# Performance work log

Measured on AMD Instinct MI355X. Metric: run time of the kernel, lower is better.

The kernel has to match this reference:

```python
import jax, jax.numpy as jnp
import numpy as np

B = 2048
D = 256
TEMPERATURE = 0.5
EPS = 1e-8  # torch.nn.CosineSimilarity eps


def _neg_indices(b):
    # Static mask: exclude diagonal and positive pairs (i, B+i), (B+i, i).
    n = 2 * b
    mask = np.ones((n, n), dtype=bool)
    np.fill_diagonal(mask, False)
    idx = np.arange(b)
    mask[idx, b + idx] = False
    mask[b + idx, idx] = False
    rows, cols = np.nonzero(mask)  # row-major order, matches torch sim[mask]
    return rows.reshape(n, n - 2), cols.reshape(n, n - 2)

_NEG_ROWS, _NEG_COLS = _neg_indices(B)


def setup_inputs() -> dict:
    key = jax.random.key(0)
    k1, k2 = jax.random.split(key)
    z_i = jax.random.normal(k1, (B, D), dtype=jnp.float32)
    z_j = jax.random.normal(k2, (B, D), dtype=jnp.float32)
    return {"z_i": z_i, "z_j": z_j}


def reference(z_i, z_j):
    b = z_i.shape[0]
    n = 2 * b
    z = jnp.concatenate([z_i, z_j], axis=0)  # [N, D]
    # Cosine similarity = normalize -> matmul (same math as broadcast CosineSimilarity)
    norm = jnp.maximum(jnp.linalg.norm(z, axis=1, keepdims=True), EPS)
    zn = z / norm
    sim = (zn @ zn.T) / TEMPERATURE  # [N, N]
    # positives: diag(sim, B) and diag(sim, -B)
    pos = jnp.concatenate([jnp.diagonal(sim, offset=b), jnp.diagonal(sim, offset=-b)], axis=0)  # [N]
    # negatives: static masked gather -> [N, N-2]
    neg = sim[_NEG_ROWS, _NEG_COLS]
    logits = jnp.concatenate([pos[:, None], neg], axis=1)  # [N, N-1]
    # CrossEntropyLoss(reduction='sum') with labels all zero, then / N
    loss = -jax.nn.log_softmax(logits, axis=1)[:, 0]
    return jnp.sum(loss) / n
```

## Files before the change

### kernel.cpp

```cpp
#include <hip/hip_runtime.h>
#include <hip/hip_bf16.h>
#include <math.h>

#define B_PAIRS 2048
#define N_ROWS  4096
#define D_DIM   256
#define INV_T   2.0f

typedef __attribute__((ext_vector_type(8))) short  short8;
typedef __attribute__((ext_vector_type(4))) float  floatx4;


__device__ __forceinline__ void async_copy16(const void* gsrc, void* ldst) {
    __builtin_amdgcn_global_load_lds(
        (__attribute__((address_space(1))) void*)gsrc,
        (__attribute__((address_space(3))) void*)ldst,
        16, 0, 0);
}

__global__ void ntx_normalize(const float* __restrict__ z_i,
                              const float* __restrict__ z_j,
                              __hip_bfloat16* __restrict__ zn) {
    const int row = blockIdx.x;
    const int tid = threadIdx.x;
    const float* src = (row < B_PAIRS) ? (z_i + (size_t)row * D_DIM)
                                       : (z_j + (size_t)(row - B_PAIRS) * D_DIM);
    float v  = src[tid];
    float ss = v * v;
    #pragma unroll
    for (int off = 32; off > 0; off >>= 1) ss += __shfl_down(ss, off, 64);
    __shared__ float red[4];
    const int lane = tid & 63, w = tid >> 6;
    if (lane == 0) red[w] = ss;
    __syncthreads();
    if (tid == 0) red[0] = red[0] + red[1] + red[2] + red[3];
    __syncthreads();
    float norm = fmaxf(sqrtf(red[0]), 1e-8f);
    zn[(size_t)row * D_DIM + tid] = __float2bfloat16(v / norm);
}

#define BM 128
#define BN 128
#define BK 32

__global__ __launch_bounds__(256)
void ntx_simtile(const __hip_bfloat16* __restrict__ zn,
                 float* __restrict__ S,
                 float* __restrict__ pos) {
    __shared__ __align__(16) __hip_bfloat16 As[BM * BK];
    __shared__ __align__(16) __hip_bfloat16 Bs[BN * BK];

    const int tid  = threadIdx.x;
    const int lane = tid & 63;
    const int w    = tid >> 6;
    const int wr   = w >> 1;
    const int wc   = w & 1;
    const int quad = lane >> 4;
    const int l16  = lane & 15;

    const int rowA0 = blockIdx.y * BM;
    const int rowB0 = blockIdx.x * BN;

    floatx4 acc[4][4];
    #pragma unroll
    for (int i = 0; i < 4; i++)
        #pragma unroll
        for (int j = 0; j < 4; j++)
            acc[i][j] = (floatx4){0.f, 0.f, 0.f, 0.f};

    for (int k0 = 0; k0 < D_DIM; k0 += BK) {
        #pragma unroll
        for (int c = 0; c < 2; c++) {
            const int chunk = tid + c * 256;
            const int r  = chunk >> 2;
            const int kc = chunk & 3;
            async_copy16(zn + ((size_t)(rowA0 + r) * D_DIM + k0 + kc * 8),
                         As + chunk * 8);
            async_copy16(zn + ((size_t)(rowB0 + r) * D_DIM + k0 + kc * 8),
                         Bs + chunk * 8);
        }
        __syncthreads();

        short8 afr[4], bfr[4];
        #pragma unroll
        for (int fi = 0; fi < 4; fi++) {
            const int ar = wr * 64 + fi * 16 + l16;
            afr[fi] = *(const short8*)(const void*)(As + ar * BK + quad * 8);
        }
        #pragma unroll
        for (int fj = 0; fj < 4; fj++) {
            const int brw = wc * 64 + fj * 16 + l16;
            bfr[fj] = *(const short8*)(const void*)(Bs + brw * BK + quad * 8);
        }
        #pragma unroll
        for (int fi = 0; fi < 4; fi++)
            #pragma unroll
            for (int fj = 0; fj < 4; fj++)
                acc[fi][fj] = __builtin_amdgcn_mfma_f32_16x16x32_bf16(
                    afr[fi], bfr[fj], acc[fi][fj], 0, 0, 0);
        __syncthreads();
    }

    #pragma unroll
    for (int fi = 0; fi < 4; fi++) {
        float rs[4] = {0.f, 0.f, 0.f, 0.f};
        #pragma unroll
        for (int fj = 0; fj < 4; fj++) {
            const int jg = rowB0 + wc * 64 + fj * 16 + l16;
            #pragma unroll
            for (int reg = 0; reg < 4; reg++) {
                const int ig = rowA0 + wr * 64 + fi * 16 + quad * 4 + reg;
                const float v = acc[fi][fj][reg] * INV_T;
                if (jg == (ig ^ B_PAIRS)) pos[ig] = v;
                rs[reg] += (jg == ig) ? 0.f : __expf(v);
            }
        }
        #pragma unroll
        for (int reg = 0; reg < 4; reg++) {
            float r = rs[reg];
            r += __shfl_xor(r, 1, 16);
            r += __shfl_xor(r, 2, 16);
            r += __shfl_xor(r, 4, 16);
            r += __shfl_xor(r, 8, 16);
            if (l16 == 0) {
                const int ig = rowA0 + wr * 64 + fi * 16 + quad * 4 + reg;
                atomicAdd(&S[ig], r);
            }
        }
    }
}

__global__ void ntx_finalize(const float* __restrict__ S,
                             const float* __restrict__ pos,
                             float* __restrict__ out) {
    const int tid = threadIdx.x;
    float acc = 0.f;
    for (int i = tid; i < N_ROWS; i += 256)
        acc += logf(S[i]) - pos[i];
    #pragma unroll
    for (int off = 32; off > 0; off >>= 1) acc += __shfl_down(acc, off, 64);
    __shared__ float red[4];
    if ((tid & 63) == 0) red[tid >> 6] = acc;
    __syncthreads();
    if (tid == 0)
        out[0] = (red[0] + red[1] + red[2] + red[3]) / (float)N_ROWS;
}

extern "C" void kernel_launch(void* const* d_in, const int* in_sizes, int n_in,
                              void* d_out, int out_size, void* d_ws, size_t ws_size,
                              hipStream_t stream) {
    const float* z_i = (const float*)d_in[0];
    const float* z_j = (const float*)d_in[1];
    float* out = (float*)d_out;

    __hip_bfloat16* zn = (__hip_bfloat16*)d_ws;
    float* S   = (float*)((char*)d_ws + (size_t)N_ROWS * D_DIM * sizeof(__hip_bfloat16));
    float* pos = S + N_ROWS;

    hipMemsetAsync(S, 0, N_ROWS * sizeof(float), stream);

    ntx_normalize<<<N_ROWS, D_DIM, 0, stream>>>(z_i, z_j, zn);

    dim3 grid(N_ROWS / BN, N_ROWS / BM);
    ntx_simtile<<<grid, 256, 0, stream>>>(zn, S, pos);

    ntx_finalize<<<1, 256, 0, stream>>>(S, pos, out);
}
```

Before: 94.56 us.

## Exploit similarity symmetry with upper-triangular tiles and fold memset into normalize

The similarity tile kernel now runs only the 528 upper-triangular tiles of the symmetric sim matrix. Each off-diagonal tile adds its exp values to both the row sums and the column sums, which roughly halves the MFMA and exp work. The normalize kernel handles one row per wavefront with float4 loads and also zeroes S, so the separate memset launch is gone. Finalize uses 1024 threads and fast log. The costs are more atomics per tile (column sums on top of row sums) and a serial loop at block start that decodes the tile index.

Result: faster. 81.48 us (-13.8%).

```diff
diff --git a/kernel.cpp b/kernel.cpp
--- a/kernel.cpp
+++ b/kernel.cpp
@@ -18,30 +18,34 @@
         16, 0, 0);
 }
 
-__global__ void ntx_normalize(const float* __restrict__ z_i,
-                              const float* __restrict__ z_j,
-                              __hip_bfloat16* __restrict__ zn) {
-    const int row = blockIdx.x;
-    const int tid = threadIdx.x;
+__global__ __launch_bounds__(256)
+void ntx_normalize(const float* __restrict__ z_i,
+                   const float* __restrict__ z_j,
+                   __hip_bfloat16* __restrict__ zn,
+                   float* __restrict__ S) {
+    const int w    = threadIdx.x >> 6;
+    const int lane = threadIdx.x & 63;
+    const int row  = blockIdx.x * 4 + w;
     const float* src = (row < B_PAIRS) ? (z_i + (size_t)row * D_DIM)
                                        : (z_j + (size_t)(row - B_PAIRS) * D_DIM);
-    float v  = src[tid];
-    float ss = v * v;
+    const float4 v = *(const float4*)(src + lane * 4);
+    float ss = v.x * v.x + v.y * v.y + v.z * v.z + v.w * v.w;
     #pragma unroll
-    for (int off = 32; off > 0; off >>= 1) ss += __shfl_down(ss, off, 64);
-    __shared__ float red[4];
-    const int lane = tid & 63, w = tid >> 6;
-    if (lane == 0) red[w] = ss;
-    __syncthreads();
-    if (tid == 0) red[0] = red[0] + red[1] + red[2] + red[3];
-    __syncthreads();
-    float norm = fmaxf(sqrtf(red[0]), 1e-8f);
-    zn[(size_t)row * D_DIM + tid] = __float2bfloat16(v / norm);
+    for (int off = 32; off > 0; off >>= 1) ss += __shfl_xor(ss, off, 64);
+    const float rn = 1.0f / fmaxf(sqrtf(ss), 1e-8f);
+    union { short4 s4; __hip_bfloat16 h[4]; } u;
+    u.h[0] = __float2bfloat16(v.x * rn);
+    u.h[1] = __float2bfloat16(v.y * rn);
+    u.h[2] = __float2bfloat16(v.z * rn);
+    u.h[3] = __float2bfloat16(v.w * rn);
+    *(short4*)(void*)(zn + (size_t)row * D_DIM + lane * 4) = u.s4;
+    if (lane == 0) S[row] = 0.0f;
 }
 
 #define BM 128
 #define BN 128
 #define BK 32
+#define N_TILES 528
 
 __global__ __launch_bounds__(256)
 void ntx_simtile(const __hip_bfloat16* __restrict__ zn,
@@ -49,6 +53,10 @@
                  float* __restrict__ pos) {
     __shared__ __align__(16) __hip_bfloat16 As[BM * BK];
     __shared__ __align__(16) __hip_bfloat16 Bs[BN * BK];
+
+    int t = blockIdx.x, by = 0, rowlen = 32;
+    while (t >= rowlen) { t -= rowlen; by++; rowlen--; }
+    const int bx = by + t;
 
     const int tid  = threadIdx.x;
     const int lane = tid & 63;
@@ -58,8 +66,10 @@
     const int quad = lane >> 4;
     const int l16  = lane & 15;
 
-    const int rowA0 = blockIdx.y * BM;
-    const int rowB0 = blockIdx.x * BN;
+    const int rowA0 = by * BM;
+    const int rowB0 = bx * BN;
+    const bool isDiag = (rowA0 == rowB0);
+    const bool isPos  = (rowB0 == (rowA0 ^ B_PAIRS));
 
     floatx4 acc[4][4];
     #pragma unroll
@@ -101,18 +111,25 @@
         __syncthreads();
     }
 
+    float cs[4] = {0.f, 0.f, 0.f, 0.f};
     #pragma unroll
     for (int fi = 0; fi < 4; fi++) {
         float rs[4] = {0.f, 0.f, 0.f, 0.f};
         #pragma unroll
         for (int fj = 0; fj < 4; fj++) {
-            const int jg = rowB0 + wc * 64 + fj * 16 + l16;
+            const int rj = wc * 64 + fj * 16 + l16;
             #pragma unroll
             for (int reg = 0; reg < 4; reg++) {
-                const int ig = rowA0 + wr * 64 + fi * 16 + quad * 4 + reg;
+                const int ri = wr * 64 + fi * 16 + quad * 4 + reg;
                 const float v = acc[fi][fj][reg] * INV_T;
-                if (jg == (ig ^ B_PAIRS)) pos[ig] = v;
-                rs[reg] += (jg == ig) ? 0.f : __expf(v);
+                const bool d = (ri == rj);
+                if (isPos && d) {
+                    pos[rowA0 + ri] = v;
+                    pos[rowB0 + rj] = v;
+                }
+                const float e = (isDiag && d) ? 0.f : __expf(v);
+                rs[reg] += e;
+                cs[fj]  += e;
             }
         }
         #pragma unroll
@@ -122,28 +139,44 @@
             r += __shfl_xor(r, 2, 16);
             r += __shfl_xor(r, 4, 16);
             r += __shfl_xor(r, 8, 16);
-            if (l16 == 0) {
-                const int ig = rowA0 + wr * 64 + fi * 16 + quad * 4 + reg;
-                atomicAdd(&S[ig], r);
-            }
+            if (l16 == 0)
+                atomicAdd(&S[rowA0 + wr * 64 + fi * 16 + quad * 4 + reg], r);
+        }
+    }
+    if (!isDiag) {
+        #pragma unroll
+        for (int fj = 0; fj < 4; fj++) {
+            float c = cs[fj];
+            c += __shfl_xor(c, 16, 64);
+            c += __shfl_xor(c, 32, 64);
+            if (quad == 0)
+                atomicAdd(&S[rowB0 + wc * 64 + fj * 16 + l16], c);
         }
     }
 }
 
-__global__ void ntx_finalize(const float* __restrict__ S,
-                             const float* __restrict__ pos,
-                             float* __restrict__ out) {
+__global__ __launch_bounds__(1024)
+void ntx_finalize(const float* __restrict__ S,
+                  const float* __restrict__ pos,
+                  float* __restrict__ out) {
     const int tid = threadIdx.x;
     float acc = 0.f;
-    for (int i = tid; i < N_ROWS; i += 256)
-        acc += logf(S[i]) - pos[i];
+    #pragma unroll
+    for (int c = 0; c < 4; c++) {
+        const int i = tid + c * 1024;
+        acc += __logf(S[i]) - pos[i];
+    }
     #pragma unroll
     for (int off = 32; off > 0; off >>= 1) acc += __shfl_down(acc, off, 64);
-    __shared__ float red[4];
+    __shared__ float red[16];
     if ((tid & 63) == 0) red[tid >> 6] = acc;
     __syncthreads();
-    if (tid == 0)
-        out[0] = (red[0] + red[1] + red[2] + red[3]) / (float)N_ROWS;
+    if (tid == 0) {
+        float s = 0.f;
+        #pragma unroll
+        for (int k = 0; k < 16; k++) s += red[k];
+        out[0] = s / (float)N_ROWS;
+    }
 }
 
 extern "C" void kernel_launch(void* const* d_in, const int* in_sizes, int n_in,
@@ -157,12 +190,7 @@
     float* S   = (float*)((char*)d_ws + (size_t)N_ROWS * D_DIM * sizeof(__hip_bfloat16));
     float* pos = S + N_ROWS;
 
-    hipMemsetAsync(S, 0, N_ROWS * sizeof(float), stream);
-
-    ntx_normalize<<<N_ROWS, D_DIM, 0, stream>>>(z_i, z_j, zn);
-
-    dim3 grid(N_ROWS / BN, N_ROWS / BM);
-    ntx_simtile<<<grid, 256, 0, stream>>>(zn, S, pos);
-
-    ntx_finalize<<<1, 256, 0, stream>>>(S, pos, out);
+    ntx_normalize<<<N_ROWS / 4, 256, 0, stream>>>(z_i, z_j, zn, S);
+    ntx_simtile<<<N_TILES, 256, 0, stream>>>(zn, S, pos);
+    ntx_finalize<<<1, 1024, 0, stream>>>(S, pos, out);
 }
```
